# Kernel tuning notes

Measured on AMD Instinct MI355X. Metric: run time of the kernel, lower is better.

The kernel has to match this reference:

```python
import jax, jax.numpy as jnp
import numpy as np

D_MSA = 256
D_PAIR = 128
N_HEADS = 8
HEAD_DIM = D_MSA // N_HEADS
EPS = 1e-5


def setup_inputs() -> dict:
    key = jax.random.key(0)
    ks = jax.random.split(key, 14)
    s = 0.02
    return {
        "msa": jax.random.normal(ks[0], (1, 64, 256, D_MSA), dtype=jnp.float32),
        "pair": jax.random.normal(ks[1], (1, 256, 256, D_PAIR), dtype=jnp.float32),
        "Wq": jax.random.normal(ks[2], (D_MSA, D_MSA), dtype=jnp.float32) * s,
        "bq": jnp.zeros((D_MSA,), jnp.float32),
        "Wk": jax.random.normal(ks[3], (D_MSA, D_MSA), dtype=jnp.float32) * s,
        "bk": jnp.zeros((D_MSA,), jnp.float32),
        "Wv": jax.random.normal(ks[4], (D_MSA, D_MSA), dtype=jnp.float32) * s,
        "bv": jnp.zeros((D_MSA,), jnp.float32),
        "Wpb": jax.random.normal(ks[5], (D_PAIR, N_HEADS), dtype=jnp.float32) * s,
        "bpb": jnp.zeros((N_HEADS,), jnp.float32),
        "Wo": jax.random.normal(ks[6], (D_MSA, D_MSA), dtype=jnp.float32) * s,
        "bo": jnp.zeros((D_MSA,), jnp.float32),
        "gamma": jnp.ones((D_MSA,), jnp.float32),
        "beta": jnp.zeros((D_MSA,), jnp.float32),
    }


def reference(msa, pair, Wq, bq, Wk, bk, Wv, bv, Wpb, bpb, Wo, bo, gamma, beta):
    B, N, L, D = msa.shape
    H, Hd = N_HEADS, HEAD_DIM
    # projections -> (B, N, L, H, Hd)
    q = (msa @ Wq + bq).reshape(B, N, L, H, Hd)
    k = (msa @ Wk + bk).reshape(B, N, L, H, Hd)
    v = (msa @ Wv + bv).reshape(B, N, L, H, Hd)
    # scores: (B, N, H, L, L)
    scores = jnp.einsum('bnihd,bnjhd->bnhij', q, k) / jnp.sqrt(jnp.float32(Hd))
    # pair bias: (B, L, L, H) -> (B, H, L, L), broadcast over N
    pb = jnp.transpose(pair @ Wpb + bpb, (0, 3, 1, 2))
    scores = scores + pb[:, None]
    attn = jax.nn.softmax(scores, axis=-1)
    attn_out = jnp.einsum('bnhij,bnjhd->bnihd', attn, v).reshape(B, N, L, D)
    attn_out = attn_out @ Wo + bo
    # residual + LayerNorm
    x = msa + attn_out
    mu = jnp.mean(x, axis=-1, keepdims=True)
    var = jnp.var(x, axis=-1, keepdims=True)
    return (x - mu) * jax.lax.rsqrt(var + EPS) * gamma + beta
```

## Files before the change

### kernel.cpp

```cpp
#include <hip/hip_runtime.h>

#define NSEQ 64
#define LL   256
#define DD   256
#define HH   8
#define HDIM 32

typedef short short8  __attribute__((ext_vector_type(8)));
typedef short short4v __attribute__((ext_vector_type(4)));
typedef float float4v __attribute__((ext_vector_type(4)));

#define MFMA16(a,b,c) __builtin_amdgcn_mfma_f32_16x16x32_bf16((a),(b),(c),0,0,0)

__device__ __forceinline__ float4v zero4() {
  float4v z;
  z[0] = 0.f; z[1] = 0.f; z[2] = 0.f; z[3] = 0.f;
  return z;
}

__device__ __forceinline__ short f2b(float f) {
  unsigned u = __float_as_uint(f);
  u = (u + 0x7fffu + ((u >> 16) & 1u)) >> 16;
  return (short)u;
}

__device__ __forceinline__ float b2f(short s) {
  return __uint_as_float(((unsigned)(unsigned short)s) << 16);
}

__device__ __forceinline__ short8 cvt8(const float* p) {
  float4 a = *(const float4*)p;
  float4 b = *(const float4*)(p + 4);
  short8 r;
  r[0] = f2b(a.x); r[1] = f2b(a.y); r[2] = f2b(a.z); r[3] = f2b(a.w);
  r[4] = f2b(b.x); r[5] = f2b(b.y); r[6] = f2b(b.z); r[7] = f2b(b.w);
  return r;
}

__device__ __forceinline__ void ld_lds16(const void* g, void* l) {
  __builtin_amdgcn_global_load_lds(
      (const __attribute__((address_space(1))) unsigned int*)g,
      (__attribute__((address_space(3))) unsigned int*)l, 16, 0, 0);
}
#define WAIT_VM0() __builtin_amdgcn_s_waitcnt(0x0F70)

#define WT_OFF    0
#define PB_OFF    (4*65536*2)
#define PBF_OFF   (PB_OFF + 8*65536*2)
#define Q_OFF     (PB_OFF + 8*65536*4)
#define K_OFF     (Q_OFF  + 16384*256*2)
#define VT_OFF    (K_OFF  + 16384*256*2)
#define MSA16_OFF (VT_OFF + 16384*256*2)
#define O_OFF     MSA16_OFF

__global__ __launch_bounds__(256) void k1_prep(
    const float* __restrict__ msa,  const float* __restrict__ pair,
    const float* __restrict__ Wq,   const float* __restrict__ Wk,
    const float* __restrict__ Wv,   const float* __restrict__ Wpb,
    const float* __restrict__ bpb,  const float* __restrict__ Wo,
    char* __restrict__ ws)
{
  __shared__ short ldsWt[16 * 136];
  int bx = blockIdx.x, tid = threadIdx.x;
  if (bx < 256) {
    short* pb16 = (short*)(ws + PB_OFF);
    for (int i = tid; i < 16 * 136; i += 256) ldsWt[i] = 0;
    __syncthreads();
    {
      float4 wv4 = *(const float4*)&Wpb[tid * 4];
      int kk = (tid * 4) >> 3, n0 = (tid * 4) & 7;
      ldsWt[(n0 + 0) * 136 + kk] = f2b(wv4.x);
      ldsWt[(n0 + 1) * 136 + kk] = f2b(wv4.y);
      ldsWt[(n0 + 2) * 136 + kk] = f2b(wv4.z);
      ldsWt[(n0 + 3) * 136 + kk] = f2b(wv4.w);
    }
    __syncthreads();
    int w = tid >> 6, l = tid & 63, q = l >> 4, c = l & 15;
    int base = bx * 256 + w * 64;
    float bias = bpb[c & 7];
    short8 bf[4];
#pragma unroll
    for (int ks = 0; ks < 4; ks++)
      bf[ks] = *(const short8*)&ldsWt[c * 136 + ks * 32 + q * 8];
    float4v acc[4];
#pragma unroll
    for (int mt = 0; mt < 4; mt++) acc[mt] = zero4();
#pragma unroll
    for (int ks = 0; ks < 4; ks++) {
#pragma unroll
      for (int mt = 0; mt < 4; mt++) {
        short8 af = cvt8(&pair[(base + mt * 16 + c) * 128 + ks * 32 + q * 8]);
        acc[mt] = MFMA16(af, bf[ks], acc[mt]);
      }
    }
    if (c < 8) {
#pragma unroll
      for (int mt = 0; mt < 4; mt++) {
        short4v o;
#pragma unroll
        for (int r = 0; r < 4; r++) o[r] = f2b(acc[mt][r] + bias);
        *(short4v*)&pb16[c * 65536 + base + mt * 16 + q * 4] = o;
      }
    }
  } else if (bx < 1280) {
    int b2 = bx - 256;
    int mat = b2 >> 8, r = b2 & 255;
    const float* W = (mat == 0) ? Wq : (mat == 1) ? Wk : (mat == 2) ? Wv : Wo;
    short* wt = (short*)(ws + WT_OFF) + mat * 65536;
    wt[tid * 256 + r] = f2b(W[r * 256 + tid]);
  } else {
    int b3 = bx - 1280;
    const float* src = msa + b3 * 8192;
    short* dst = (short*)(ws + MSA16_OFF) + b3 * 8192;
#pragma unroll
    for (int i = 0; i < 8; i++) {
      int idx = i * 1024 + tid * 4;
      float4 v = *(const float4*)&src[idx];
      short4v s;
      s[0] = f2b(v.x); s[1] = f2b(v.y); s[2] = f2b(v.z); s[3] = f2b(v.w);
      *(short4v*)&dst[idx] = s;
    }
  }
}

__global__ __launch_bounds__(256) void k2_qkv(
    const float* __restrict__ bq, const float* __restrict__ bk,
    const float* __restrict__ bv, char* __restrict__ ws)
{
  __shared__ __align__(16) short lsA[128 * 128];
  __shared__ __align__(16) short lsB[128 * 128];
  int bx = blockIdx.x, tid = threadIdx.x;
  if (bx >= 768) {
    int b = bx - 768;
    int it16 = b & 15;
    const short* src = (const short*)(ws + PB_OFF) + (b >> 4) * 65536 + it16 * 4096;
    short* pbf = (short*)(ws + PBF_OFF);
    short* lt = lsA;
#pragma unroll
    for (int i2 = 0; i2 < 2; i2++) {
      int idx = i2 * 2048 + tid * 8;
      *(short8*)&lt[(idx >> 8) * 264 + (idx & 255)] = *(const short8*)&src[idx];
    }
    __syncthreads();
#pragma unroll
    for (int i2 = 0; i2 < 4; i2++) {
      int fid = i2 * 256 + tid;
      int jt = fid >> 6, lane = fid & 63;
      int qp = lane >> 4, cp = lane & 15;
      short4v v;
#pragma unroll
      for (int r = 0; r < 4; r++)
        v[r] = lt[(qp * 4 + r) * 264 + jt * 16 + cp];
      *(short4v*)&pbf[((b * 16 + jt) * 64 + lane) * 4] = v;
    }
    return;
  }
  int rt = bx & 127, ct = bx >> 7;
  int m = ct >> 1, cb = (ct & 1) * 128;
  int R0 = rt * 128;
  const short* msa16 = (const short*)(ws + MSA16_OFF);
  const short* wt = (const short*)(ws + WT_OFF) + m * 65536;
  int w = tid >> 6, l = tid & 63, q = l >> 4, c = l & 15;
  int WR = (w & 1) * 64, WC = (w >> 1) * 64;
  float4v acc[4][4];
#pragma unroll
  for (int mt = 0; mt < 4; mt++)
#pragma unroll
    for (int nt = 0; nt < 4; nt++) acc[mt][nt] = zero4();

#pragma unroll 1
  for (int kk = 0; kk < 2; kk++) {
    if (kk) __syncthreads();
#pragma unroll
    for (int i = 0; i < 8; i++) {
      int ci = i * 256 + tid;
      int r = ci >> 4, pos = ci & 15;
      int kc = pos ^ (r & 7);
      ld_lds16(&msa16[(R0 + r) * 256 + kk * 128 + kc * 8], &lsA[ci * 8]);
    }
#pragma unroll
    for (int i = 0; i < 8; i++) {
      int ci = i * 256 + tid;
      int r = ci >> 4, pos = ci & 15;
      int kc = pos ^ (r & 7);
      ld_lds16(&wt[(cb + r) * 256 + kk * 128 + kc * 8], &lsB[ci * 8]);
    }
    WAIT_VM0();
    __syncthreads();
#pragma unroll
    for (int ks = 0; ks < 4; ks++) {
      short8 af[4], bf[4];
#pragma unroll
      for (int mt = 0; mt < 4; mt++) {
        int r = WR + mt * 16 + c;
        int phys = (ks * 4 + q) ^ (r & 7);
        af[mt] = *(const short8*)&lsA[r * 128 + phys * 8];
      }
#pragma unroll
      for (int nt = 0; nt < 4; nt++) {
        int r = WC + nt * 16 + c;
        int phys = (ks * 4 + q) ^ (r & 7);
        bf[nt] = *(const short8*)&lsB[r * 128 + phys * 8];
      }
#pragma unroll
      for (int mt = 0; mt < 4; mt++)
#pragma unroll
        for (int nt = 0; nt < 4; nt++)
          acc[mt][nt] = MFMA16(af[mt], bf[nt], acc[mt][nt]);
    }
  }

  const float* bp = (m == 0) ? bq : (m == 1) ? bk : bv;
  int n = R0 >> 8;
  if (m < 2) {
    short* dst = (short*)(ws + (m == 0 ? Q_OFF : K_OFF));
#pragma unroll
    for (int nt = 0; nt < 4; nt++) {
      int ch = cb + WC + nt * 16 + c;
      float bb = bp[ch];
      int h = ch >> 5, hd = ch & 31;
#pragma unroll
      for (int mt = 0; mt < 4; mt++) {
        int i0 = (R0 & 255) + WR + mt * 16 + q * 4;
#pragma unroll
        for (int r = 0; r < 4; r++)
          dst[((n * HH + h) * 256 + i0 + r) * HDIM + hd] = f2b(acc[mt][nt][r] + bb);
      }
    }
  } else {
    short* vt = (short*)(ws + VT_OFF);
#pragma unroll
    for (int nt = 0; nt < 4; nt++) {
      int ch = cb + WC + nt * 16 + c;
      float bb = bp[ch];
#pragma unroll
      for (int mt = 0; mt < 4; mt++) {
        int j0 = (R0 & 255) + WR + mt * 16 + q * 4;
        short4v s4;
#pragma unroll
        for (int r = 0; r < 4; r++) s4[r] = f2b(acc[mt][nt][r] + bb);
        *(short4v*)&vt[((n * HH + (ch >> 5)) * HDIM + (ch & 31)) * 256 + j0] = s4;
      }
    }
  }
}

__global__ __launch_bounds__(256) void k3_attn(char* __restrict__ ws)
{
  __shared__ short P[64 * 264];
  int bx = blockIdx.x, tid = threadIdx.x;
  int qq = bx >> 9, grp = bx & 511;
  int n = grp >> 3, h = grp & 7;
  int w = tid >> 6, l = tid & 63, q = l >> 4, c = l & 15;
  const short* qh = (const short*)(ws + Q_OFF) + (n * HH + h) * 256 * HDIM;
  const short* kh = (const short*)(ws + K_OFF) + (n * HH + h) * 256 * HDIM;
  const short* vt = (const short*)(ws + VT_OFF) + (n * HH + h) * HDIM * 256;
  const short* pbf = (const short*)(ws + PBF_OFF) + (h * 16 + qq * 4 + w) * 16 * 256;
  short* os = (short*)(ws + O_OFF);
  const float scale = 0.17677669529663687f;
  int i0 = qq * 64 + w * 16;
  short8 aq = *(const short8*)&qh[(i0 + c) * HDIM + q * 8];
  float4v s[16];
#pragma unroll
  for (int jt = 0; jt < 16; jt++) {
    short8 bk8 = *(const short8*)&kh[(jt * 16 + c) * HDIM + q * 8];
    s[jt] = MFMA16(aq, bk8, zero4());
  }
#pragma unroll
  for (int jt = 0; jt < 16; jt++) {
    short4v pv = *(const short4v*)&pbf[(jt * 64 + l) * 4];
#pragma unroll
    for (int r = 0; r < 4; r++)
      s[jt][r] = __builtin_fmaf(s[jt][r], scale, b2f(pv[r]));
  }
  float inv[4];
#pragma unroll
  for (int r = 0; r < 4; r++) {
    float m = s[0][r];
#pragma unroll
    for (int jt = 1; jt < 16; jt++) m = fmaxf(m, s[jt][r]);
    m = fmaxf(m, __shfl_xor(m, 1, 64));
    m = fmaxf(m, __shfl_xor(m, 2, 64));
    m = fmaxf(m, __shfl_xor(m, 4, 64));
    m = fmaxf(m, __shfl_xor(m, 8, 64));
    float rs = 0.f;
#pragma unroll
    for (int jt = 0; jt < 16; jt++) {
      float p = __expf(s[jt][r] - m);
      s[jt][r] = p;
      rs += p;
    }
    rs += __shfl_xor(rs, 1, 64);
    rs += __shfl_xor(rs, 2, 64);
    rs += __shfl_xor(rs, 4, 64);
    rs += __shfl_xor(rs, 8, 64);
    inv[r] = 1.f / rs;
  }
#pragma unroll
  for (int jt = 0; jt < 16; jt++)
#pragma unroll
    for (int r = 0; r < 4; r++)
      P[(w * 16 + q * 4 + r) * 264 + jt * 16 + c] = f2b(s[jt][r]);
  float4v o0 = zero4(), o1 = zero4();
#pragma unroll
  for (int kk = 0; kk < 8; kk++) {
    short8 ap = *(const short8*)&P[(w * 16 + c) * 264 + kk * 32 + q * 8];
    short8 b0 = *(const short8*)&vt[c * 256 + kk * 32 + q * 8];
    short8 b1 = *(const short8*)&vt[(16 + c) * 256 + kk * 32 + q * 8];
    o0 = MFMA16(ap, b0, o0);
    o1 = MFMA16(ap, b1, o1);
  }
#pragma unroll
  for (int r = 0; r < 4; r++) {
    os[(n * 256 + i0 + q * 4 + r) * 256 + h * 32 + c]      = f2b(o0[r] * inv[r]);
    os[(n * 256 + i0 + q * 4 + r) * 256 + h * 32 + 16 + c] = f2b(o1[r] * inv[r]);
  }
}

__global__ __launch_bounds__(256) void k4_out(
    const float* __restrict__ msa, const float* __restrict__ bo,
    const float* __restrict__ gamma, const float* __restrict__ beta,
    const char* __restrict__ ws, float* __restrict__ out)
{
  __shared__ __align__(16) short lsA[64 * 128];
  __shared__ __align__(16) short lsB[256 * 128];
  int bx = blockIdx.x, tid = threadIdx.x;
  int w = tid >> 6, l = tid & 63, q = l >> 4, c = l & 15;
  int R0 = bx * 64;
  const short* osrc = (const short*)(ws + O_OFF);
  const short* wto  = (const short*)(ws + WT_OFF) + 3 * 65536;
  float4v acc[16];
#pragma unroll
  for (int nt = 0; nt < 16; nt++) acc[nt] = zero4();

#pragma unroll 1
  for (int kk = 0; kk < 2; kk++) {
    if (kk) __syncthreads();
#pragma unroll
    for (int i = 0; i < 4; i++) {
      int ci = i * 256 + tid;
      int r = ci >> 4, pos = ci & 15;
      int kc = pos ^ (r & 7);
      ld_lds16(&osrc[(R0 + r) * 256 + kk * 128 + kc * 8], &lsA[ci * 8]);
    }
#pragma unroll
    for (int i = 0; i < 16; i++) {
      int ci = i * 256 + tid;
      int r = ci >> 4, pos = ci & 15;
      int kc = pos ^ (r & 7);
      ld_lds16(&wto[r * 256 + kk * 128 + kc * 8], &lsB[ci * 8]);
    }
    WAIT_VM0();
    __syncthreads();
#pragma unroll
    for (int ks = 0; ks < 4; ks++) {
      int rA = w * 16 + c;
      int physA = (ks * 4 + q) ^ (rA & 7);
      short8 af = *(const short8*)&lsA[rA * 128 + physA * 8];
#pragma unroll
      for (int nt = 0; nt < 16; nt++) {
        int r = nt * 16 + c;
        int phys = (ks * 4 + q) ^ (r & 7);
        short8 bf = *(const short8*)&lsB[r * 128 + phys * 8];
        acc[nt] = MFMA16(af, bf, acc[nt]);
      }
    }
  }

  int r0 = R0 + w * 16;
  float s1[4] = {0, 0, 0, 0}, s2[4] = {0, 0, 0, 0};
#pragma unroll
  for (int nt = 0; nt < 16; nt++) {
    float bb = bo[nt * 16 + c];
#pragma unroll
    for (int r = 0; r < 4; r++) {
      float x = acc[nt][r] + bb + msa[(r0 + q * 4 + r) * 256 + nt * 16 + c];
      acc[nt][r] = x;
      s1[r] += x;
      s2[r] = __builtin_fmaf(x, x, s2[r]);
    }
  }
  float mu[4], rsd[4];
#pragma unroll
  for (int r = 0; r < 4; r++) {
    float a = s1[r], b = s2[r];
    a += __shfl_xor(a, 1, 64); b += __shfl_xor(b, 1, 64);
    a += __shfl_xor(a, 2, 64); b += __shfl_xor(b, 2, 64);
    a += __shfl_xor(a, 4, 64); b += __shfl_xor(b, 4, 64);
    a += __shfl_xor(a, 8, 64); b += __shfl_xor(b, 8, 64);
    float m = a * (1.f / 256.f);
    float v = __builtin_fmaf(-m, m, b * (1.f / 256.f));
    mu[r] = m;
    rsd[r] = rsqrtf(v + 1e-5f);
  }
#pragma unroll
  for (int nt = 0; nt < 16; nt++) {
    float g = gamma[nt * 16 + c], bt = beta[nt * 16 + c];
#pragma unroll
    for (int r = 0; r < 4; r++)
      out[(r0 + q * 4 + r) * 256 + nt * 16 + c] =
          (acc[nt][r] - mu[r]) * rsd[r] * g + bt;
  }
}

extern "C" void kernel_launch(void* const* d_in, const int* in_sizes, int n_in,
                              void* d_out, int out_size, void* d_ws, size_t ws_size,
                              hipStream_t stream)
{
  const float* msa   = (const float*)d_in[0];
  const float* pair  = (const float*)d_in[1];
  const float* Wq    = (const float*)d_in[2];
  const float* bq    = (const float*)d_in[3];
  const float* Wk    = (const float*)d_in[4];
  const float* bk    = (const float*)d_in[5];
  const float* Wv    = (const float*)d_in[6];
  const float* bv    = (const float*)d_in[7];
  const float* Wpb   = (const float*)d_in[8];
  const float* bpb   = (const float*)d_in[9];
  const float* Wo    = (const float*)d_in[10];
  const float* bo    = (const float*)d_in[11];
  const float* gamma = (const float*)d_in[12];
  const float* beta  = (const float*)d_in[13];
  char* ws = (char*)d_ws;
  float* out = (float*)d_out;

  hipLaunchKernelGGL(k1_prep, dim3(1792), dim3(256), 0, stream,
                     msa, pair, Wq, Wk, Wv, Wpb, bpb, Wo, ws);
  hipLaunchKernelGGL(k2_qkv, dim3(896), dim3(256), 0, stream,
                     bq, bk, bv, ws);
  hipLaunchKernelGGL(k3_attn, dim3(2048), dim3(256), 0, stream, ws);
  hipLaunchKernelGGL(k4_out, dim3(256), dim3(256), 0, stream,
                     msa, bo, gamma, beta, ws, out);
}
```

Baseline: 177.3 us.

## Split output projection across column halves and read operands directly from global

The output-projection plus LayerNorm kernel now uses 32 rows per block, with two waves per 16-row group each handling half of the 256 output columns. Grid size doubles to 512 blocks. The LDS staging of the attention output and Wo tiles is removed, and MFMA operands are loaded straight from global memory, relying on L2/cache for Wo reuse. The LayerNorm row statistics are combined across the two column halves through a small shared array and one barrier. This aims to raise parallelism and cut LDS traffic and barriers, at the cost of uncoalesced, repeated global loads of Wo.

```diff
diff --git a/kernel.cpp b/kernel.cpp
--- a/kernel.cpp
+++ b/kernel.cpp
@@ -322,83 +322,73 @@
     const float* __restrict__ gamma, const float* __restrict__ beta,
     const char* __restrict__ ws, float* __restrict__ out)
 {
-  __shared__ __align__(16) short lsA[64 * 128];
-  __shared__ __align__(16) short lsB[256 * 128];
+  __shared__ float sred[2][32][2];
   int bx = blockIdx.x, tid = threadIdx.x;
   int w = tid >> 6, l = tid & 63, q = l >> 4, c = l & 15;
-  int R0 = bx * 64;
+  int rg = w >> 1, ch2 = w & 1;
+  int R0 = bx * 32 + rg * 16;
+  int C0 = ch2 * 128;
   const short* osrc = (const short*)(ws + O_OFF);
   const short* wto  = (const short*)(ws + WT_OFF) + 3 * 65536;
-  float4v acc[16];
-#pragma unroll
-  for (int nt = 0; nt < 16; nt++) acc[nt] = zero4();
-
-#pragma unroll 1
-  for (int kk = 0; kk < 2; kk++) {
-    if (kk) __syncthreads();
-#pragma unroll
-    for (int i = 0; i < 4; i++) {
-      int ci = i * 256 + tid;
-      int r = ci >> 4, pos = ci & 15;
-      int kc = pos ^ (r & 7);
-      ld_lds16(&osrc[(R0 + r) * 256 + kk * 128 + kc * 8], &lsA[ci * 8]);
-    }
-#pragma unroll
-    for (int i = 0; i < 16; i++) {
-      int ci = i * 256 + tid;
-      int r = ci >> 4, pos = ci & 15;
-      int kc = pos ^ (r & 7);
-      ld_lds16(&wto[r * 256 + kk * 128 + kc * 8], &lsB[ci * 8]);
-    }
-    WAIT_VM0();
-    __syncthreads();
-#pragma unroll
-    for (int ks = 0; ks < 4; ks++) {
-      int rA = w * 16 + c;
-      int physA = (ks * 4 + q) ^ (rA & 7);
-      short8 af = *(const short8*)&lsA[rA * 128 + physA * 8];
-#pragma unroll
-      for (int nt = 0; nt < 16; nt++) {
-        int r = nt * 16 + c;
-        int phys = (ks * 4 + q) ^ (r & 7);
-        short8 bf = *(const short8*)&lsB[r * 128 + phys * 8];
-        acc[nt] = MFMA16(af, bf, acc[nt]);
-      }
-    }
-  }
-
-  int r0 = R0 + w * 16;
+
+  float4v acc[8];
+#pragma unroll
+  for (int nt = 0; nt < 8; nt++) acc[nt] = zero4();
+
+#pragma unroll
+  for (int ks = 0; ks < 8; ks++) {
+    short8 af = *(const short8*)&osrc[(R0 + c) * 256 + ks * 32 + q * 8];
+#pragma unroll
+    for (int nt = 0; nt < 8; nt++) {
+      short8 bf = *(const short8*)&wto[(C0 + nt * 16 + c) * 256 + ks * 32 + q * 8];
+      acc[nt] = MFMA16(af, bf, acc[nt]);
+    }
+  }
+
   float s1[4] = {0, 0, 0, 0}, s2[4] = {0, 0, 0, 0};
 #pragma unroll
-  for (int nt = 0; nt < 16; nt++) {
-    float bb = bo[nt * 16 + c];
+  for (int nt = 0; nt < 8; nt++) {
+    float bb = bo[C0 + nt * 16 + c];
 #pragma unroll
     for (int r = 0; r < 4; r++) {
-      float x = acc[nt][r] + bb + msa[(r0 + q * 4 + r) * 256 + nt * 16 + c];
+      float x = acc[nt][r] + bb + msa[(R0 + q * 4 + r) * 256 + C0 + nt * 16 + c];
       acc[nt][r] = x;
       s1[r] += x;
       s2[r] = __builtin_fmaf(x, x, s2[r]);
     }
   }
+#pragma unroll
+  for (int r = 0; r < 4; r++) {
+    s1[r] += __shfl_xor(s1[r], 1, 64); s2[r] += __shfl_xor(s2[r], 1, 64);
+    s1[r] += __shfl_xor(s1[r], 2, 64); s2[r] += __shfl_xor(s2[r], 2, 64);
+    s1[r] += __shfl_xor(s1[r], 4, 64); s2[r] += __shfl_xor(s2[r], 4, 64);
+    s1[r] += __shfl_xor(s1[r], 8, 64); s2[r] += __shfl_xor(s2[r], 8, 64);
+  }
+  if (c == 0) {
+#pragma unroll
+    for (int r = 0; r < 4; r++) {
+      sred[0][rg * 16 + q * 4 + r][ch2] = s1[r];
+      sred[1][rg * 16 + q * 4 + r][ch2] = s2[r];
+    }
+  }
+  __syncthreads();
   float mu[4], rsd[4];
 #pragma unroll
   for (int r = 0; r < 4; r++) {
-    float a = s1[r], b = s2[r];
-    a += __shfl_xor(a, 1, 64); b += __shfl_xor(b, 1, 64);
-    a += __shfl_xor(a, 2, 64); b += __shfl_xor(b, 2, 64);
-    a += __shfl_xor(a, 4, 64); b += __shfl_xor(b, 4, 64);
-    a += __shfl_xor(a, 8, 64); b += __shfl_xor(b, 8, 64);
+    int row = rg * 16 + q * 4 + r;
+    float a = sred[0][row][0] + sred[0][row][1];
+    float b = sred[1][row][0] + sred[1][row][1];
     float m = a * (1.f / 256.f);
     float v = __builtin_fmaf(-m, m, b * (1.f / 256.f));
     mu[r] = m;
     rsd[r] = rsqrtf(v + 1e-5f);
   }
 #pragma unroll
-  for (int nt = 0; nt < 16; nt++) {
-    float g = gamma[nt * 16 + c], bt = beta[nt * 16 + c];
+  for (int nt = 0; nt < 8; nt++) {
+    float g = gamma[C0 + nt * 16 + c], bt = beta[C0 + nt * 16 + c];
 #pragma unroll
     for (int r = 0; r < 4; r++)
-      out[(r0 + q * 4 + r) * 256 + nt * 16 + c] =
+      out[(R0 + q * 4 + r) * 256 + C0 + nt * 16 + c] =
           (acc[nt][r] - mu[r]) * rsd[r] * g + bt;
   }
 }
@@ -429,6 +419,6 @@
   hipLaunchKernelGGL(k2_qkv, dim3(896), dim3(256), 0, stream,
                      bq, bk, bv, ws);
   hipLaunchKernelGGL(k3_attn, dim3(2048), dim3(256), 0, stream, ws);
-  hipLaunchKernelGGL(k4_out, dim3(256), dim3(256), 0, stream,
+  hipLaunchKernelGGL(k4_out, dim3(512), dim3(256), 0, stream,
                      msa, bo, gamma, beta, ws, out);
 }
```

Measured after the change: 187.7 us. 1.06x slower.
